# Performance work log

Hardware: AMD Instinct MI355X
Metric: run time of the kernel (lower is better)

## Reference

```python
import jax, jax.numpy as jnp
import numpy as np

W = 128
POS_FREQ = 10  # -> 3*10*2 = 60 encoded dims
VIEW_FREQ = 4  # -> 3*4*2 = 24 encoded dims


def freq_encode(v, n_freq):
    # tcnn 'Frequency' encoding: sin/cos of 2^j * pi * x per input dim.
    scales = (2.0 ** jnp.arange(n_freq, dtype=v.dtype)) * jnp.pi  # [F]
    ang = v[..., :, None] * scales  # [N, 3, F]
    enc = jnp.stack([jnp.sin(ang), jnp.cos(ang)], axis=-1)  # [N, 3, F, 2]
    return enc.reshape(v.shape[0], -1)  # [N, 3*F*2]


def mlp(h, weights):
    # tcnn FullyFusedMLP: bias-free, ReLU on hidden layers, linear output.
    for Wm in weights[:-1]:
        h = jax.nn.relu(h @ Wm)
    return h @ weights[-1]


def setup_inputs():
    key = jax.random.key(0)
    ks = jax.random.split(key, 10)
    N = 1048576

    def w(k, fan_in, fan_out):
        s = (1.0 / np.sqrt(fan_in)).astype(np.float32)
        return jax.random.uniform(k, (fan_in, fan_out), jnp.float32, -s, s)

    return {
        "x": jax.random.uniform(ks[0], (N, 6), jnp.float32),
        "Wd1_0": w(ks[1], 60, W),
        "Wd1_1": w(ks[2], W, W),
        "Wd1_2": w(ks[3], W, W),
        "Wd2_0": w(ks[4], 60 + W, W),
        "Wd2_1": w(ks[5], W, W),
        "Wd2_2": w(ks[6], W, W),
        "Wd2_3": w(ks[7], W, W + 1),
        "Wc_0": w(ks[8], 24 + W, W),
        "Wc_1": w(ks[9], W, 3),
    }


def reference(x, Wd1_0, Wd1_1, Wd1_2, Wd2_0, Wd2_1, Wd2_2, Wd2_3, Wc_0, Wc_1):
    pos, view = x[:, :3], x[:, 3:6]
    # Density MLP
    enc_pos = freq_encode(pos, POS_FREQ)                # [N, 60]
    part1 = mlp(enc_pos, [Wd1_0, Wd1_1, Wd1_2])          # [N, 128]
    dens_out = mlp(jnp.concatenate([enc_pos, part1], -1),
                   [Wd2_0, Wd2_1, Wd2_2, Wd2_3])         # [N, 129]
    blending = jax.nn.sigmoid(dens_out[:, :1])           # [N, 1]
    feature = dens_out[:, 1:]                            # [N, 128]
    density = feature[:, 0:1]                            # [N, 1]
    # Color MLP
    enc_view = freq_encode(view, VIEW_FREQ)              # [N, 24]
    rgb = mlp(jnp.concatenate([enc_view, feature], -1), [Wc_0, Wc_1])  # [N, 3]
    return jnp.concatenate([rgb, density, blending], -1)  # [N, 5]
```

## Files before the change

kernel.cpp:

```cpp
#include <hip/hip_runtime.h>
#include <cstdint>
#include <cstddef>

typedef __attribute__((ext_vector_type(8))) __bf16 bf16x8;
typedef __attribute__((ext_vector_type(16))) float floatx16;

struct SrcPtrs { const float* p[9]; };


__global__ void prep_zero(unsigned short* __restrict__ ws) {
  uint4* p = (uint4*)ws;
  const int n = 143360 / 8;
  for (int i = blockIdx.x * blockDim.x + threadIdx.x; i < n; i += gridDim.x * blockDim.x)
    p[i] = make_uint4(0u, 0u, 0u, 0u);
}

__global__ void prep_fill(SrcPtrs sp, unsigned short* __restrict__ ws) {
  const int m  = blockIdx.x >> 4;
  const int sl = blockIdx.x & 15;
  const int K[9]  = {60, 128, 128, 188, 128, 128, 128, 152, 128};
  const int N[9]  = {128, 128, 128, 128, 128, 128, 129, 128, 3};
  const int SS[9] = {4, 8, 8, 12, 8, 8, 8, 10, 8};
  const unsigned OFF[9] = {0u, 8192u, 24576u, 40960u, 65536u, 81920u, 98304u, 118784u, 139264u};
  const int Km = K[m], Nm = N[m], Sm = SS[m];
  const float* __restrict__ src = sp.p[m];
  unsigned short* __restrict__ dst = ws + OFF[m];
  const int tot = Km * Nm;
  for (int i = sl * 256 + (int)threadIdx.x; i < tot; i += 16 * 256) {
    int k = i / Nm;
    int n = i - k * Nm;
    int kk = k, row = n;
    if (m == 3) kk = (k < 60) ? 128 + k : k - 60;
    if (m == 7) kk = (k < 24) ? 128 + k : k - 24;
    if (m == 6) row = (n == 0) ? 128 : n - 1;
    const int t = row >> 5, l31 = row & 31;
    const int s = kk >> 4, q2 = (kk >> 3) & 1, j = kk & 7;
    dst[(t * Sm + s) * 512 + (q2 * 32 + l31) * 8 + j] =
        __builtin_bit_cast(unsigned short, (__bf16)src[i]);
  }
}


#if defined(__has_builtin)
#if __has_builtin(__builtin_amdgcn_permlane32_swap)
#define HAVE_PLSWAP 1
#endif
#endif
#ifndef HAVE_PLSWAP
#define HAVE_PLSWAP 0
#endif

__device__ __forceinline__ unsigned pk2(float a, float b) {
  unsigned short ua = __builtin_bit_cast(unsigned short, (__bf16)a);
  unsigned short ub = __builtin_bit_cast(unsigned short, (__bf16)b);
  return (unsigned)ua | ((unsigned)ub << 16);
}

__device__ __forceinline__ void stage16(const void* g, void* l) {
  __builtin_amdgcn_global_load_lds(
      (const __attribute__((address_space(1))) unsigned int*)g,
      (__attribute__((address_space(3))) unsigned int*)l, 16, 0, 0);
}

__device__ __forceinline__ void half_swap(unsigned a, unsigned b, int q2,
                                          unsigned& lo, unsigned& hi) {
#if HAVE_PLSWAP
  auto r = __builtin_amdgcn_permlane32_swap(a, b, false, false);
  lo = r[0]; hi = r[1];
#else
  unsigned sa = __shfl_xor(a, 32, 64);
  unsigned sb = __shfl_xor(b, 32, 64);
  lo = q2 ? sb : a;
  hi = q2 ? b : sa;
#endif
}

template <int KIND>
__device__ __forceinline__ bf16x8 trig_frag(const float (&x)[6], int q2, int sl) {
  bf16x8 r;
#pragma unroll
  for (int j = 0; j < 8; ++j) {
    const int kA = 16 * sl + j;
    const int kB = 16 * sl + 8 + j;
    int dA, dB; float scA, scB; bool vA, vB;
    if (KIND == 0) {
      vA = kA < 60; vB = kB < 60;
      dA = kA / 20; dB = kB / 20;
      scA = (float)(1 << ((kA % 20) >> 1)) * 0.5f;
      scB = (float)(1 << ((kB % 20) >> 1)) * 0.5f;
    } else {
      vA = kA < 24; vB = kB < 24;
      dA = 3 + (kA >> 3); dB = 3 + (kB >> 3);
      scA = (float)(1 << ((kA & 7) >> 1)) * 0.5f;
      scB = (float)(1 << ((kB & 7) >> 1)) * 0.5f;
    }
    float v  = q2 ? x[dB] : x[dA];
    float sc = q2 ? scB : scA;
    bool ok  = q2 ? vB : vA;
    float rev = v * sc;
    float t = (j & 1) ? __builtin_amdgcn_cosf(rev) : __builtin_amdgcn_sinf(rev);
    r[j] = (__bf16)(ok ? t : 0.0f);
  }
  return r;
}

template <int S, int SL, int NT, int HT, int PP, bool RELU, int OUTM>
__device__ __forceinline__ void run_layer(const unsigned short* __restrict__ wsrc,
                                          const unsigned short* __restrict__ nsrc, int nbytes,
                                          unsigned short* __restrict__ sWt,
                                          uint2 (&pkv)[2][16],
                                          const bf16x8 (&tail)[2][4],
                                          float* __restrict__ out, int base, int tid) {
  const int lane = tid & 63;
  const int w = tid >> 6;
  const int q2 = lane >> 5;
  const int l31 = lane & 31;
  const int pt0 = base + w * 64 + l31;
  const int pt1 = pt0 + 32;

  __syncthreads();

  if (nbytes > 0) {
    const uint4* __restrict__ s4 = (const uint4*)nsrc;
    uint4* __restrict__ dst = (uint4*)(sWt + (PP ^ 1) * 12288);
    const int n16 = nbytes / 16;
    for (int i = tid; i < n16; i += 256)
      stage16(s4 + i, dst + (i & ~63));
  }

  bf16x8 bf[2][SL > 0 ? SL : 1];
#pragma unroll
  for (int s = 0; s < SL; ++s) {
#pragma unroll
    for (int m = 0; m < 2; ++m) {
      uint2 p0 = pkv[m][2 * s], p1 = pkv[m][2 * s + 1];
      unsigned w0, w1, w2, w3;
      half_swap(p0.x, p1.x, q2, w0, w2);
      half_swap(p0.y, p1.y, q2, w1, w3);
      uint4 u = make_uint4(w0, w1, w2, w3);
      bf[m][s] = __builtin_bit_cast(bf16x8, u);
    }
  }

  const unsigned short* __restrict__ ldsbuf = sWt + PP * 12288;
  const uint4* __restrict__ wp = (const uint4*)wsrc;
#pragma unroll
  for (int t = 0; t < NT; ++t) {
    floatx16 acc[2];
#pragma unroll
    for (int i = 0; i < 16; ++i) { acc[0][i] = 0.0f; acc[1][i] = 0.0f; }
#pragma unroll
    for (int s = 0; s < S; ++s) {
      bf16x8 A;
      if (t < HT) {
        A = *(const bf16x8*)&ldsbuf[(t * S + s) * 512 + lane * 8];
      } else {
        uint4 a4 = wp[(t * S + s) * 64 + lane];
        A = __builtin_bit_cast(bf16x8, a4);
      }
      bf16x8 B0 = (s < SL) ? bf[0][s < SL ? s : 0] : tail[0][s - SL];
      bf16x8 B1 = (s < SL) ? bf[1][s < SL ? s : 0] : tail[1][s - SL];
      acc[0] = __builtin_amdgcn_mfma_f32_32x32x16_bf16(A, B0, acc[0], 0, 0, 0);
      acc[1] = __builtin_amdgcn_mfma_f32_32x32x16_bf16(A, B1, acc[1], 0, 0, 0);
    }
    if (OUTM == 2) {
      if (q2 == 0) {
        float* o0 = out + (size_t)pt0 * 5;
        o0[0] = acc[0][0]; o0[1] = acc[0][1]; o0[2] = acc[0][2];
        float* o1 = out + (size_t)pt1 * 5;
        o1[0] = acc[1][0]; o1[1] = acc[1][1]; o1[2] = acc[1][2];
      }
    } else {
      if (OUTM == 0 || t < 4) {
#pragma unroll
        for (int m = 0; m < 2; ++m) {
#pragma unroll
          for (int gg = 0; gg < 4; ++gg) {
            float b0 = acc[m][4 * gg], b1 = acc[m][4 * gg + 1];
            float b2 = acc[m][4 * gg + 2], b3 = acc[m][4 * gg + 3];
            if (RELU) {
              b0 = fmaxf(b0, 0.f); b1 = fmaxf(b1, 0.f);
              b2 = fmaxf(b2, 0.f); b3 = fmaxf(b3, 0.f);
            }
            pkv[m][4 * t + gg] = make_uint2(pk2(b0, b1), pk2(b2, b3));
          }
        }
      }
      if (OUTM == 1 && q2 == 0) {
        if (t == 0) {
          out[(size_t)pt0 * 5 + 3] = acc[0][0];
          out[(size_t)pt1 * 5 + 3] = acc[1][0];
        }
        if (t == 4) {
          out[(size_t)pt0 * 5 + 4] = 1.0f / (1.0f + __expf(-acc[0][0]));
          out[(size_t)pt1 * 5 + 4] = 1.0f / (1.0f + __expf(-acc[1][0]));
        }
      }
    }
  }
}

__global__ __launch_bounds__(256, 2) void nerf_main(const float* __restrict__ x,
                                                    const unsigned short* __restrict__ ws,
                                                    float* __restrict__ out) {
  __shared__ __align__(16) unsigned short sWt[2 * 12288];

  const int tid = (int)threadIdx.x;
  const int base = (int)blockIdx.x * 256;
  const int lane = tid & 63;
  const int w = tid >> 6;
  const int q2 = lane >> 5;
  const int l31 = lane & 31;
  const int pt0 = base + w * 64 + l31;

  {
    const uint4* s4 = (const uint4*)ws;
    uint4* dst = (uint4*)sWt;
#pragma unroll
    for (int i = 0; i < 2; ++i)
      stage16(s4 + i * 256 + tid, dst + ((i * 256 + tid) & ~63));
  }

  float x0[6], x1[6];
  {
    const float* a = x + (size_t)pt0 * 6;
    const float* b = x + (size_t)(pt0 + 32) * 6;
#pragma unroll
    for (int c = 0; c < 3; ++c) {
      float2 u = *(const float2*)(a + 2 * c);
      float2 v = *(const float2*)(b + 2 * c);
      x0[2 * c] = u.x; x0[2 * c + 1] = u.y;
      x1[2 * c] = v.x; x1[2 * c + 1] = v.y;
    }
  }

  bf16x8 pkt[2][4];
#pragma unroll
  for (int sl = 0; sl < 4; ++sl) {
    pkt[0][sl] = trig_frag<0>(x0, q2, sl);
    pkt[1][sl] = trig_frag<0>(x1, q2, sl);
  }

  uint2 pkv[2][16];

  run_layer< 4, 0, 4, 2, 0, true , 0>(ws + 0u,      ws + 8192u,   16384, sWt, pkv, pkt, out, base, tid);
  run_layer< 8, 8, 4, 2, 1, true , 0>(ws + 8192u,   ws + 24576u,  16384, sWt, pkv, pkt, out, base, tid);
  run_layer< 8, 8, 4, 2, 0, false, 0>(ws + 24576u,  ws + 40960u,  24576, sWt, pkv, pkt, out, base, tid);
  run_layer<12, 8, 4, 2, 1, true , 0>(ws + 40960u,  ws + 65536u,  16384, sWt, pkv, pkt, out, base, tid);
  run_layer< 8, 8, 4, 2, 0, true , 0>(ws + 65536u,  ws + 81920u,  16384, sWt, pkv, pkt, out, base, tid);
  run_layer< 8, 8, 4, 2, 1, true , 0>(ws + 81920u,  ws + 98304u,  24576, sWt, pkv, pkt, out, base, tid);
  run_layer< 8, 8, 5, 3, 0, false, 1>(ws + 98304u,  ws + 118784u, 20480, sWt, pkv, pkt, out, base, tid);

  bf16x8 vw[2][4];
#pragma unroll
  for (int sl = 0; sl < 2; ++sl) {
    vw[0][sl] = trig_frag<1>(x0, q2, sl);
    vw[1][sl] = trig_frag<1>(x1, q2, sl);
  }
  vw[0][2] = vw[0][0]; vw[0][3] = vw[0][0];
  vw[1][2] = vw[1][0]; vw[1][3] = vw[1][0];

  run_layer<10, 8, 4, 2, 1, true , 0>(ws + 118784u, ws + 139264u,  8192, sWt, pkv, vw,  out, base, tid);
  run_layer< 8, 8, 1, 1, 0, false, 2>(ws + 139264u, (const unsigned short*)nullptr, 0, sWt, pkv, pkt, out, base, tid);
}

extern "C" void kernel_launch(void* const* d_in, const int* in_sizes, int n_in,
                              void* d_out, int out_size, void* d_ws, size_t ws_size,
                              hipStream_t stream) {
  (void)n_in; (void)out_size; (void)ws_size;
  const float* x = (const float*)d_in[0];
  SrcPtrs sp;
  for (int i = 0; i < 9; ++i) sp.p[i] = (const float*)d_in[1 + i];
  unsigned short* ws = (unsigned short*)d_ws;
  float* out = (float*)d_out;
  const int N = in_sizes[0] / 6;

  prep_zero<<<70, 256, 0, stream>>>(ws);
  prep_fill<<<144, 256, 0, stream>>>(sp, ws);
  nerf_main<<<N / 256, 256, 0, stream>>>(x, ws, out);
}
```

Baseline: 359.7 us.

## Permute weight K-layout so MFMA outputs feed next layer without lane swaps

Weights are re-laid out with bits 2 and 3 of the K index swapped, and the trig encoding order is permuted to match. The packed bf16 activations from one layer's MFMA accumulator can then be used directly as the next layer's B operand, with no cross-half permlane or shuffle swaps. It also double-buffers the activation registers (ping-pong P0/P1), makes the staging loop compile-time unrolled, and starts each accumulation from a shared zero accumulator. The risks are higher register pressure from the two activation buffers and subtle layout mismatches that would break correctness.

```diff
diff --git a/kernel.cpp b/kernel.cpp
--- a/kernel.cpp
+++ b/kernel.cpp
@@ -33,6 +33,7 @@
     if (m == 3) kk = (k < 60) ? 128 + k : k - 60;
     if (m == 7) kk = (k < 24) ? 128 + k : k - 24;
     if (m == 6) row = (n == 0) ? 128 : n - 1;
+    kk = (kk & ~12) | (((kk & 4) << 1) | ((kk & 8) >> 1));
     const int t = row >> 5, l31 = row & 31;
     const int s = kk >> 4, q2 = (kk >> 3) & 1, j = kk & 7;
     dst[(t * Sm + s) * 512 + (q2 * 32 + l31) * 8 + j] =
@@ -41,15 +42,6 @@
 }
 
 
-#if defined(__has_builtin)
-#if __has_builtin(__builtin_amdgcn_permlane32_swap)
-#define HAVE_PLSWAP 1
-#endif
-#endif
-#ifndef HAVE_PLSWAP
-#define HAVE_PLSWAP 0
-#endif
-
 __device__ __forceinline__ unsigned pk2(float a, float b) {
   unsigned short ua = __builtin_bit_cast(unsigned short, (__bf16)a);
   unsigned short ub = __builtin_bit_cast(unsigned short, (__bf16)b);
@@ -62,26 +54,13 @@
       (__attribute__((address_space(3))) unsigned int*)l, 16, 0, 0);
 }
 
-__device__ __forceinline__ void half_swap(unsigned a, unsigned b, int q2,
-                                          unsigned& lo, unsigned& hi) {
-#if HAVE_PLSWAP
-  auto r = __builtin_amdgcn_permlane32_swap(a, b, false, false);
-  lo = r[0]; hi = r[1];
-#else
-  unsigned sa = __shfl_xor(a, 32, 64);
-  unsigned sb = __shfl_xor(b, 32, 64);
-  lo = q2 ? sb : a;
-  hi = q2 ? b : sa;
-#endif
-}
-
 template <int KIND>
 __device__ __forceinline__ bf16x8 trig_frag(const float (&x)[6], int q2, int sl) {
   bf16x8 r;
 #pragma unroll
   for (int j = 0; j < 8; ++j) {
-    const int kA = 16 * sl + j;
-    const int kB = 16 * sl + 8 + j;
+    const int kA = 16 * sl + j + (j >= 4 ? 4 : 0);
+    const int kB = kA + 4;
     int dA, dB; float scA, scB; bool vA, vB;
     if (KIND == 0) {
       vA = kA < 60; vB = kB < 60;
@@ -104,12 +83,14 @@
   return r;
 }
 
-template <int S, int SL, int NT, int HT, int PP, bool RELU, int OUTM>
+template <int S, int SL, int NT, int HT, int PP, bool RELU, int OUTM, int NB>
 __device__ __forceinline__ void run_layer(const unsigned short* __restrict__ wsrc,
-                                          const unsigned short* __restrict__ nsrc, int nbytes,
+                                          const unsigned short* __restrict__ nsrc,
                                           unsigned short* __restrict__ sWt,
-                                          uint2 (&pkv)[2][16],
+                                          const uint4 (&pin)[2][8],
+                                          uint4 (&pout)[2][8],
                                           const bf16x8 (&tail)[2][4],
+                                          floatx16 ZACC,
                                           float* __restrict__ out, int base, int tid) {
   const int lane = tid & 63;
   const int w = tid >> 6;
@@ -120,25 +101,13 @@
 
   __syncthreads();
 
-  if (nbytes > 0) {
+  if (NB > 0) {
     const uint4* __restrict__ s4 = (const uint4*)nsrc;
     uint4* __restrict__ dst = (uint4*)(sWt + (PP ^ 1) * 12288);
-    const int n16 = nbytes / 16;
-    for (int i = tid; i < n16; i += 256)
+#pragma unroll
+    for (int kI = 0; kI < NB / (16 * 256); ++kI) {
+      const int i = kI * 256 + tid;
       stage16(s4 + i, dst + (i & ~63));
-  }
-
-  bf16x8 bf[2][SL > 0 ? SL : 1];
-#pragma unroll
-  for (int s = 0; s < SL; ++s) {
-#pragma unroll
-    for (int m = 0; m < 2; ++m) {
-      uint2 p0 = pkv[m][2 * s], p1 = pkv[m][2 * s + 1];
-      unsigned w0, w1, w2, w3;
-      half_swap(p0.x, p1.x, q2, w0, w2);
-      half_swap(p0.y, p1.y, q2, w1, w3);
-      uint4 u = make_uint4(w0, w1, w2, w3);
-      bf[m][s] = __builtin_bit_cast(bf16x8, u);
     }
   }
 
@@ -147,8 +116,6 @@
 #pragma unroll
   for (int t = 0; t < NT; ++t) {
     floatx16 acc[2];
-#pragma unroll
-    for (int i = 0; i < 16; ++i) { acc[0][i] = 0.0f; acc[1][i] = 0.0f; }
 #pragma unroll
     for (int s = 0; s < S; ++s) {
       bf16x8 A;
@@ -158,10 +125,17 @@
         uint4 a4 = wp[(t * S + s) * 64 + lane];
         A = __builtin_bit_cast(bf16x8, a4);
       }
-      bf16x8 B0 = (s < SL) ? bf[0][s < SL ? s : 0] : tail[0][s - SL];
-      bf16x8 B1 = (s < SL) ? bf[1][s < SL ? s : 0] : tail[1][s - SL];
-      acc[0] = __builtin_amdgcn_mfma_f32_32x32x16_bf16(A, B0, acc[0], 0, 0, 0);
-      acc[1] = __builtin_amdgcn_mfma_f32_32x32x16_bf16(A, B1, acc[1], 0, 0, 0);
+      bf16x8 B0 = (s < SL) ? __builtin_bit_cast(bf16x8, pin[0][(s < SL) ? s : 0])
+                           : tail[0][s - SL];
+      bf16x8 B1 = (s < SL) ? __builtin_bit_cast(bf16x8, pin[1][(s < SL) ? s : 0])
+                           : tail[1][s - SL];
+      if (s == 0) {
+        acc[0] = __builtin_amdgcn_mfma_f32_32x32x16_bf16(A, B0, ZACC, 0, 0, 0);
+        acc[1] = __builtin_amdgcn_mfma_f32_32x32x16_bf16(A, B1, ZACC, 0, 0, 0);
+      } else {
+        acc[0] = __builtin_amdgcn_mfma_f32_32x32x16_bf16(A, B0, acc[0], 0, 0, 0);
+        acc[1] = __builtin_amdgcn_mfma_f32_32x32x16_bf16(A, B1, acc[1], 0, 0, 0);
+      }
     }
     if (OUTM == 2) {
       if (q2 == 0) {
@@ -182,7 +156,14 @@
               b0 = fmaxf(b0, 0.f); b1 = fmaxf(b1, 0.f);
               b2 = fmaxf(b2, 0.f); b3 = fmaxf(b3, 0.f);
             }
-            pkv[m][4 * t + gg] = make_uint2(pk2(b0, b1), pk2(b2, b3));
+            const unsigned lo = pk2(b0, b1), hi = pk2(b2, b3);
+            if ((gg & 1) == 0) {
+              pout[m][2 * t + (gg >> 1)].x = lo;
+              pout[m][2 * t + (gg >> 1)].y = hi;
+            } else {
+              pout[m][2 * t + (gg >> 1)].z = lo;
+              pout[m][2 * t + (gg >> 1)].w = hi;
+            }
           }
         }
       }
@@ -241,15 +222,19 @@
     pkt[1][sl] = trig_frag<0>(x1, q2, sl);
   }
 
-  uint2 pkv[2][16];
-
-  run_layer< 4, 0, 4, 2, 0, true , 0>(ws + 0u,      ws + 8192u,   16384, sWt, pkv, pkt, out, base, tid);
-  run_layer< 8, 8, 4, 2, 1, true , 0>(ws + 8192u,   ws + 24576u,  16384, sWt, pkv, pkt, out, base, tid);
-  run_layer< 8, 8, 4, 2, 0, false, 0>(ws + 24576u,  ws + 40960u,  24576, sWt, pkv, pkt, out, base, tid);
-  run_layer<12, 8, 4, 2, 1, true , 0>(ws + 40960u,  ws + 65536u,  16384, sWt, pkv, pkt, out, base, tid);
-  run_layer< 8, 8, 4, 2, 0, true , 0>(ws + 65536u,  ws + 81920u,  16384, sWt, pkv, pkt, out, base, tid);
-  run_layer< 8, 8, 4, 2, 1, true , 0>(ws + 81920u,  ws + 98304u,  24576, sWt, pkv, pkt, out, base, tid);
-  run_layer< 8, 8, 5, 3, 0, false, 1>(ws + 98304u,  ws + 118784u, 20480, sWt, pkv, pkt, out, base, tid);
+  floatx16 zacc;
+#pragma unroll
+  for (int i = 0; i < 16; ++i) zacc[i] = 0.0f;
+
+  uint4 P0[2][8], P1[2][8];
+
+  run_layer< 4, 0, 4, 2, 0, true , 0, 16384>(ws + 0u,      ws + 8192u,   sWt, P0, P0, pkt, zacc, out, base, tid);
+  run_layer< 8, 8, 4, 2, 1, true , 0, 16384>(ws + 8192u,   ws + 24576u,  sWt, P0, P1, pkt, zacc, out, base, tid);
+  run_layer< 8, 8, 4, 2, 0, false, 0, 24576>(ws + 24576u,  ws + 40960u,  sWt, P1, P0, pkt, zacc, out, base, tid);
+  run_layer<12, 8, 4, 2, 1, true , 0, 16384>(ws + 40960u,  ws + 65536u,  sWt, P0, P1, pkt, zacc, out, base, tid);
+  run_layer< 8, 8, 4, 2, 0, true , 0, 16384>(ws + 65536u,  ws + 81920u,  sWt, P1, P0, pkt, zacc, out, base, tid);
+  run_layer< 8, 8, 4, 2, 1, true , 0, 24576>(ws + 81920u,  ws + 98304u,  sWt, P0, P1, pkt, zacc, out, base, tid);
+  run_layer< 8, 8, 5, 3, 0, false, 1, 20480>(ws + 98304u,  ws + 118784u, sWt, P1, P0, pkt, zacc, out, base, tid);
 
   bf16x8 vw[2][4];
 #pragma unroll
@@ -260,8 +245,8 @@
   vw[0][2] = vw[0][0]; vw[0][3] = vw[0][0];
   vw[1][2] = vw[1][0]; vw[1][3] = vw[1][0];
 
-  run_layer<10, 8, 4, 2, 1, true , 0>(ws + 118784u, ws + 139264u,  8192, sWt, pkv, vw,  out, base, tid);
-  run_layer< 8, 8, 1, 1, 0, false, 2>(ws + 139264u, (const unsigned short*)nullptr, 0, sWt, pkv, pkt, out, base, tid);
+  run_layer<10, 8, 4, 2, 1, true , 0,  8192>(ws + 118784u, ws + 139264u, sWt, P0, P1, vw,  zacc, out, base, tid);
+  run_layer< 8, 8, 1, 1, 0, false, 2,     0>(ws + 139264u, (const unsigned short*)nullptr, sWt, P1, P0, pkt, zacc, out, base, tid);
 }
 
 extern "C" void kernel_launch(void* const* d_in, const int* in_sizes, int n_in,
```

Measured after the change: 366.3 us. About the same (+1.8%).
